# Kernel tuning notes

Hardware: AMD Instinct MI355X
Metric: run time of the kernel (lower is better)

Reference implementation:

```python
import jax, jax.numpy as jnp
import numpy as np

N, E, D, C, G = 100000, 3200000, 128, 10, 512
BN_EPS = 1e-5


def setup_inputs() -> dict:
    key = jax.random.key(0)
    ks = jax.random.split(key, 16)
    s = 0.05
    return {
        "x": jax.random.normal(ks[0], (N, D), jnp.float32),
        "edge_index": jax.random.randint(ks[1], (2, E), 0, N, dtype=jnp.int64),
        "batch": jnp.sort(jax.random.randint(ks[2], (N,), 0, G, dtype=jnp.int64)),
        # 5 stacked GINConv MLPs: Linear->ReLU->Linear->ReLU->BatchNorm
        "conv_W1": jax.random.normal(ks[3], (5, D, D), jnp.float32) * s,
        "conv_b1": jnp.zeros((5, D), jnp.float32),
        "conv_W2": jax.random.normal(ks[4], (5, D, D), jnp.float32) * s,
        "conv_b2": jnp.zeros((5, D), jnp.float32),
        "conv_gamma": jnp.ones((5, D), jnp.float32),
        "conv_beta": jnp.zeros((5, D), jnp.float32),
        # fc1 / fc2: Linear->ReLU->BatchNorm (fc2 is SHARED across stages)
        "fc1_W": jax.random.normal(ks[5], (D, D), jnp.float32) * s,
        "fc1_b": jnp.zeros((D,), jnp.float32),
        "fc1_gamma": jnp.ones((D,), jnp.float32),
        "fc1_beta": jnp.zeros((D,), jnp.float32),
        "fc2_W": jax.random.normal(ks[6], (D, D), jnp.float32) * s,
        "fc2_b": jnp.zeros((D,), jnp.float32),
        "fc2_gamma": jnp.ones((D,), jnp.float32),
        "fc2_beta": jnp.zeros((D,), jnp.float32),
        "lin_W": jax.random.normal(ks[7], (D, C), jnp.float32) * s,
        "lin_b": jnp.zeros((C,), jnp.float32),
    }


def _bn(h, gamma, beta):
    # training-mode BatchNorm1d: batch stats, biased variance
    m = h.mean(axis=0)
    v = h.var(axis=0)
    return (h - m) * jax.lax.rsqrt(v + BN_EPS) * gamma + beta


def _fc(h, W, b, gamma, beta):
    return _bn(jax.nn.relu(h @ W + b), gamma, beta)


def reference(x, edge_index, batch, conv_W1, conv_b1, conv_W2, conv_b2,
              conv_gamma, conv_beta, fc1_W, fc1_b, fc1_gamma, fc1_beta,
              fc2_W, fc2_b, fc2_gamma, fc2_beta, lin_W, lin_b):
    src, dst = edge_index[0], edge_index[1]
    pool = lambda h: jax.ops.segment_sum(h, batch, num_segments=G)

    g = _fc(pool(x), fc1_W, fc1_b, fc1_gamma, fc1_beta)  # x0_g
    total = g
    h = x
    for i in range(5):
        # GINConv, eps=0: nn((1+eps)*x + sum_{j in N(i)} x_j)
        agg = jax.ops.segment_sum(h[src], dst, num_segments=N)
        z = h + agg
        z = jax.nn.relu(z @ conv_W1[i] + conv_b1[i])
        z = jax.nn.relu(z @ conv_W2[i] + conv_b2[i])
        h = _bn(z, conv_gamma[i], conv_beta[i])
        g = _fc(g + pool(h), fc2_W, fc2_b, fc2_gamma, fc2_beta)
        total = total + g
    # dropout omitted (inference); final classifier
    logits = total @ lin_W + lin_b
    return jax.nn.log_softmax(logits, axis=-1)
```

## Files before the change

### kernel.cpp

```cpp
#include <hip/hip_runtime.h>
#include <hip/hip_bf16.h>
#include <math.h>

#define D 128
#define NG 512
#define NC 10
#define PAD 96
#define CAP 704
#define BN_EPS 1e-5f

typedef __attribute__((ext_vector_type(8))) short frag_ab;
typedef __attribute__((ext_vector_type(4))) float f32x4;

__device__ __forceinline__ ushort f2bf(float v) {
    __hip_bfloat16 h = __float2bfloat16(v);
    union { __hip_bfloat16 h; ushort u; } c;
    c.h = h;
    return c.u;
}
__device__ __forceinline__ float bflo(uint u) { return __uint_as_float(u << 16); }
__device__ __forceinline__ float bfhi(uint u) { return __uint_as_float(u & 0xffff0000u); }
__device__ __forceinline__ uint packbf(float x, float y) {
    return (uint)f2bf(x) | ((uint)f2bf(y) << 16);
}

__global__ void zero_ints(int* __restrict__ p, int n) {
    int i = blockIdx.x * blockDim.x + threadIdx.x;
    int s = gridDim.x * blockDim.x;
    for (; i < n; i += s) p[i] = 0;
}

__global__ void scatter_bucket(const int* __restrict__ srcs, const int* __restrict__ dsts, int E,
                               int* __restrict__ bcnt, uint* __restrict__ ebuf) {
    int i = blockIdx.x * blockDim.x + threadIdx.x;
    int s = gridDim.x * blockDim.x;
    for (; i < E; i += s) {
        int d = dsts[i];
        int b = d >> 4;
        int pos = atomicAdd(&bcnt[b], 1);
        if (pos < CAP) ebuf[(size_t)b * CAP + pos] = (uint)srcs[i] | ((uint)(d & 15) << 24);
    }
}

__global__ void csr_phaseB(const uint* __restrict__ ebuf, const int* __restrict__ bcnt,
                           int* __restrict__ cnt, int* __restrict__ pad, int N) {
    int b = blockIdx.x;
    int tid = threadIdx.x;
    int n0 = b << 4;
    __shared__ int lcur[16];
    __shared__ int lpad[16 * PAD];
    if (tid < 16) lcur[tid] = tid * PAD;
    __syncthreads();
    int ec = bcnt[b];
    if (ec > CAP) ec = CAP;
    const uint* eb = ebuf + (size_t)b * CAP;
    for (int e = tid; e < ec; e += 256) {
        uint w = eb[e];
        int ld = w >> 24;
        int pos = atomicAdd(&lcur[ld], 1);
        if (pos < ld * PAD + PAD) lpad[pos] = (int)(w & 0x00FFFFFFu);
    }
    __syncthreads();
    int ne = N - n0;
    if (ne > 16) ne = 16;
    if (tid < ne) {
        int c = lcur[tid] - tid * PAD;
        if (c > PAD) c = PAD;
        cnt[n0 + tid] = c;
    }
    int4* dst4 = (int4*)(pad + (size_t)n0 * PAD);
    const int4* src4l = (const int4*)lpad;
    int tot4 = (ne * PAD) >> 2;
    for (int i = tid; i < tot4; i += 256) dst4[i] = src4l[i];
}

__global__ void gstart_bsearch(const int* __restrict__ batch, int N, int* __restrict__ gstart) {
    int g = blockIdx.x * blockDim.x + threadIdx.x;
    if (g > NG) return;
    if (g == NG) { gstart[NG] = N; return; }
    int lo = 0, hi = N;
    while (lo < hi) {
        int mid = (lo + hi) >> 1;
        if (batch[mid] < g) lo = mid + 1; else hi = mid;
    }
    gstart[g] = lo;
}

__global__ void cvt_bf16(const float* __restrict__ in, uint* __restrict__ out, int nPairs) {
    int i = blockIdx.x * blockDim.x + threadIdx.x;
    int s = gridDim.x * blockDim.x;
    const float2* in2 = (const float2*)in;
    for (; i < nPairs; i += s) {
        float2 v = in2[i];
        out[i] = packbf(v.x, v.y);
    }
}

__global__ void prep_w(const float* __restrict__ W1, const float* __restrict__ W2,
                       ushort* __restrict__ Wt) {
    int m = blockIdx.x;
    const float* W = (m < 5) ? (W1 + (size_t)m * D * D) : (W2 + (size_t)(m - 5) * D * D);
    ushort* out = Wt + (size_t)m * D * D;
    __shared__ ushort ws[D * D];
    int tid = threadIdx.x;
    for (int i = tid; i < D * D; i += 256) ws[i] = f2bf(W[i]);
    __syncthreads();
    int n = tid >> 1, kh = (tid & 1) << 6;
    uint* op = (uint*)(out + n * D + kh);
#pragma unroll 8
    for (int j = 0; j < 32; ++j) {
        uint lo = ws[(kh + 2 * j) * D + n];
        uint hi = ws[(kh + 2 * j + 1) * D + n];
        op[j] = lo | (hi << 16);
    }
}

#define ACC8(V) { s0 += bflo(V.x); s1 += bfhi(V.x); s2 += bflo(V.y); s3 += bfhi(V.y); \
                  s4 += bflo(V.z); s5 += bfhi(V.z); s6 += bflo(V.w); s7 += bfhi(V.w); }

__global__ void agg_pad(const uint4* __restrict__ src4, const float* __restrict__ stats,
                        const float* __restrict__ gamma, const float* __restrict__ beta,
                        float invN, const int* __restrict__ deg, const int* __restrict__ pad,
                        uint4* __restrict__ out4, int N) {
    int gtid = blockIdx.x * blockDim.x + threadIdx.x;
    int grp = gtid >> 4;
    int c16 = gtid & 15;
    int ng = (gridDim.x * blockDim.x) >> 4;
    int cb = c16 * 8;
    float A[8], B[8];
#pragma unroll
    for (int j = 0; j < 8; ++j) { A[j] = 1.f; B[j] = 0.f; }
    if (stats) {
#pragma unroll
        for (int j = 0; j < 8; ++j) {
            int c = cb + j;
            float m = stats[c] * invN;
            float v = fmaxf(stats[D + c] * invN - m * m, 0.f);
            float r = rsqrtf(v + BN_EPS);
            A[j] = r * gamma[c];
            B[j] = beta[c] - m * A[j];
        }
    }
    for (int n = grp; n < N; n += ng) {
        float s0 = 0.f, s1 = 0.f, s2 = 0.f, s3 = 0.f, s4 = 0.f, s5 = 0.f, s6 = 0.f, s7 = 0.f;
        {
            uint4 v = src4[(size_t)n * 16 + c16];
            ACC8(v);
        }
        const int* cp = pad + (size_t)n * PAD;
        int dg = deg[n];
        if (dg > PAD) dg = PAD;
        int e = 0;
        for (; e + 8 <= dg; e += 8) {
            int i0 = cp[e], i1 = cp[e + 1], i2 = cp[e + 2], i3 = cp[e + 3];
            int i4 = cp[e + 4], i5 = cp[e + 5], i6 = cp[e + 6], i7 = cp[e + 7];
            uint4 v0 = src4[(size_t)i0 * 16 + c16];
            uint4 v1 = src4[(size_t)i1 * 16 + c16];
            uint4 v2 = src4[(size_t)i2 * 16 + c16];
            uint4 v3 = src4[(size_t)i3 * 16 + c16];
            uint4 v4 = src4[(size_t)i4 * 16 + c16];
            uint4 v5 = src4[(size_t)i5 * 16 + c16];
            uint4 v6 = src4[(size_t)i6 * 16 + c16];
            uint4 v7 = src4[(size_t)i7 * 16 + c16];
            ACC8(v0); ACC8(v1); ACC8(v2); ACC8(v3);
            ACC8(v4); ACC8(v5); ACC8(v6); ACC8(v7);
        }
        for (; e < dg; ++e) {
            uint4 v0 = src4[(size_t)cp[e] * 16 + c16];
            ACC8(v0);
        }
        float db = (float)(dg + 1);
        uint4 o;
        o.x = packbf(s0 * A[0] + db * B[0], s1 * A[1] + db * B[1]);
        o.y = packbf(s2 * A[2] + db * B[2], s3 * A[3] + db * B[3]);
        o.z = packbf(s4 * A[4] + db * B[4], s5 * A[5] + db * B[5]);
        o.w = packbf(s6 * A[6] + db * B[6], s7 * A[7] + db * B[7]);
        out4[(size_t)n * 16 + c16] = o;
    }
}

__launch_bounds__(256, 2)
__global__ void gin_mlp(const uint* __restrict__ z, const ushort* __restrict__ w1t,
                        const float* __restrict__ b1, const ushort* __restrict__ w2t,
                        const float* __restrict__ b2, uint* __restrict__ outp, int N) {
    int tid = threadIdx.x;
    int lane = tid & 63;
    int wv = tid >> 6;
    int col = lane & 15;
    int kq = lane >> 4;
    int blk = blockIdx.x;
    int m0 = blk * 64 + wv * 16;
    __shared__ __align__(16) ushort cs[64 * D];

    int arow = m0 + col;
    if (arow >= N) arow = N - 1;
    const char* zrow = (const char*)z + (size_t)arow * 256 + kq * 16;
    frag_ab a0 = *(const frag_ab*)(zrow);
    frag_ab a1 = *(const frag_ab*)(zrow + 64);
    frag_ab a2 = *(const frag_ab*)(zrow + 128);
    frag_ab a3 = *(const frag_ab*)(zrow + 192);

    f32x4 acc[8];
#pragma unroll
    for (int n = 0; n < 8; ++n) {
        float bz = b1[n * 16 + col];
        acc[n] = (f32x4){bz, bz, bz, bz};
    }
    const char* wl1 = (const char*)w1t + (size_t)col * 256 + kq * 16;
#pragma unroll
    for (int kc = 0; kc < 4; ++kc) {
        frag_ab av = (kc == 0) ? a0 : (kc == 1) ? a1 : (kc == 2) ? a2 : a3;
#pragma unroll
        for (int n = 0; n < 8; ++n) {
            frag_ab bv = *(const frag_ab*)(wl1 + n * 4096 + kc * 64);
            acc[n] = __builtin_amdgcn_mfma_f32_16x16x32_bf16(av, bv, acc[n], 0, 0, 0);
        }
    }
    int rbase = wv * 16 + kq * 4;
#pragma unroll
    for (int n = 0; n < 8; ++n) {
#pragma unroll
        for (int r = 0; r < 4; ++r) {
            int row = rbase + r;
            int colo = n * 16 + col;
            int chunk = (colo >> 3) ^ (row & 15);
            cs[row * D + chunk * 8 + (colo & 7)] = f2bf(fmaxf(acc[n][r], 0.f));
        }
    }
    __syncthreads();

    int lrow = wv * 16 + col;
    frag_ab c0, c1, c2, c3;
    c0 = *(const frag_ab*)(cs + lrow * D + (((0 << 2) + kq) ^ col) * 8);
    c1 = *(const frag_ab*)(cs + lrow * D + (((1 << 2) + kq) ^ col) * 8);
    c2 = *(const frag_ab*)(cs + lrow * D + (((2 << 2) + kq) ^ col) * 8);
    c3 = *(const frag_ab*)(cs + lrow * D + (((3 << 2) + kq) ^ col) * 8);

#pragma unroll
    for (int n = 0; n < 8; ++n) {
        float bz = b2[n * 16 + col];
        acc[n] = (f32x4){bz, bz, bz, bz};
    }
    const char* wl2 = (const char*)w2t + (size_t)col * 256 + kq * 16;
#pragma unroll
    for (int kc = 0; kc < 4; ++kc) {
        frag_ab av = (kc == 0) ? c0 : (kc == 1) ? c1 : (kc == 2) ? c2 : c3;
#pragma unroll
        for (int n = 0; n < 8; ++n) {
            frag_ab bv = *(const frag_ab*)(wl2 + n * 4096 + kc * 64);
            acc[n] = __builtin_amdgcn_mfma_f32_16x16x32_bf16(av, bv, acc[n], 0, 0, 0);
        }
    }
    __syncthreads();

#pragma unroll
    for (int n = 0; n < 8; ++n) {
#pragma unroll
        for (int r = 0; r < 4; ++r) {
            int row = rbase + r;
            int colo = n * 16 + col;
            int chunk = (colo >> 3) ^ (row & 15);
            cs[row * D + chunk * 8 + (colo & 7)] = f2bf(fmaxf(acc[n][r], 0.f));
        }
    }
    __syncthreads();

    const uint4* csv = (const uint4*)cs;
    uint4* og = (uint4*)outp;
#pragma unroll
    for (int p = 0; p < 4; ++p) {
        int idx = p * 256 + tid;
        int row = idx >> 4;
        int j = idx & 15;
        uint4 v = csv[row * 16 + (j ^ (row & 15))];
        if (blk * 64 + row < N) og[(size_t)blk * 1024 + idx] = v;
    }
}

template <int BF16>
__global__ void pool_stats(const void* __restrict__ zptr, const int* __restrict__ gstart,
                           float* __restrict__ pool, float* __restrict__ stats) {
    int g = blockIdx.x;
    int tid = threadIdx.x;
    int r0 = gstart[g], r1 = gstart[g + 1];
    __shared__ float red[256];
    if (BF16) {
        const uint* z = (const uint*)zptr;
        int uc = tid & 63;
        int qq = tid >> 6;
        float s0 = 0.f, s1 = 0.f, q0 = 0.f, q1 = 0.f;
        for (int r = r0 + qq; r < r1; r += 4) {
            uint u = z[(size_t)r * 64 + uc];
            float lo = bflo(u), hi = bfhi(u);
            s0 += lo; s1 += hi;
            q0 += lo * lo; q1 += hi * hi;
        }
        float S0 = 0.f, S1 = 0.f, Q0 = 0.f, Q1 = 0.f;
        red[tid] = s0; __syncthreads();
        if (qq == 0) S0 = red[uc] + red[uc + 64] + red[uc + 128] + red[uc + 192];
        __syncthreads();
        red[tid] = s1; __syncthreads();
        if (qq == 0) S1 = red[uc] + red[uc + 64] + red[uc + 128] + red[uc + 192];
        __syncthreads();
        red[tid] = q0; __syncthreads();
        if (qq == 0) Q0 = red[uc] + red[uc + 64] + red[uc + 128] + red[uc + 192];
        __syncthreads();
        red[tid] = q1; __syncthreads();
        if (qq == 0) Q1 = red[uc] + red[uc + 64] + red[uc + 128] + red[uc + 192];
        if (qq == 0) {
            pool[g * D + 2 * uc] = S0;
            pool[g * D + 2 * uc + 1] = S1;
            if (stats) {
                atomicAdd(&stats[2 * uc], S0);
                atomicAdd(&stats[2 * uc + 1], S1);
                atomicAdd(&stats[D + 2 * uc], Q0);
                atomicAdd(&stats[D + 2 * uc + 1], Q1);
            }
        }
    } else {
        const float* z = (const float*)zptr;
        int col = tid & 127;
        int half = tid >> 7;
        float s = 0.f;
        for (int r = r0 + half; r < r1; r += 2) s += z[(size_t)r * D + col];
        red[tid] = s;
        __syncthreads();
        if (half == 0) pool[g * D + col] = red[tid] + red[tid + 128];
    }
}

__global__ void fc_forward(const float* __restrict__ pool, const float* __restrict__ stats,
                           const float* __restrict__ gamma, const float* __restrict__ beta,
                           float invN, const int* __restrict__ gstart, const float* __restrict__ gprev,
                           const float* __restrict__ W, const float* __restrict__ bias,
                           float* __restrict__ y, float* __restrict__ ystats) {
    int g = blockIdx.x;
    int tid = threadIdx.x;
    __shared__ float u[D];
    float pv = pool[g * D + tid];
    float uv;
    if (stats) {
        float m = stats[tid] * invN;
        float var = fmaxf(stats[D + tid] * invN - m * m, 0.f);
        float rs = rsqrtf(var + BN_EPS);
        float a = rs * gamma[tid];
        float b = beta[tid] - m * a;
        float cntg = (float)(gstart[g + 1] - gstart[g]);
        uv = gprev[g * D + tid] + pv * a + cntg * b;
    } else {
        uv = pv;
    }
    u[tid] = uv;
    __syncthreads();
    float acc = bias[tid];
#pragma unroll 8
    for (int k = 0; k < D; ++k) acc = fmaf(u[k], W[k * D + tid], acc);
    acc = fmaxf(acc, 0.f);
    y[g * D + tid] = acc;
    atomicAdd(&ystats[tid], acc);
    atomicAdd(&ystats[D + tid], acc * acc);
}

__global__ void fc_bn(const float* __restrict__ y, const float* __restrict__ ystats,
                      const float* __restrict__ gamma, const float* __restrict__ beta,
                      float* __restrict__ gbuf, float* __restrict__ total, int first) {
    int idx = blockIdx.x * blockDim.x + threadIdx.x;
    int d = idx & 127;
    const float invG = 1.f / NG;
    float m = ystats[d] * invG;
    float var = fmaxf(ystats[D + d] * invG - m * m, 0.f);
    float rs = rsqrtf(var + BN_EPS);
    float gv = (y[idx] - m) * rs * gamma[d] + beta[d];
    gbuf[idx] = gv;
    total[idx] = first ? gv : (total[idx] + gv);
}

__global__ void final_logits(const float* __restrict__ total, const float* __restrict__ linW,
                             const float* __restrict__ linb, float* __restrict__ out) {
    int g = blockIdx.x;
    int tid = threadIdx.x;
    __shared__ float t[D];
    __shared__ float lg[12];
    t[tid] = total[g * D + tid];
    __syncthreads();
    if (tid < NC) {
        float a = linb[tid];
        for (int k = 0; k < D; ++k) a = fmaf(t[k], linW[k * NC + tid], a);
        lg[tid] = a;
    }
    __syncthreads();
    if (tid == 0) {
        float mx = lg[0];
        for (int c = 1; c < NC; ++c) mx = fmaxf(mx, lg[c]);
        float se = 0.f;
        for (int c = 0; c < NC; ++c) se += expf(lg[c] - mx);
        lg[10] = mx + logf(se);
    }
    __syncthreads();
    if (tid < NC) out[g * NC + tid] = lg[tid] - lg[10];
}

extern "C" void kernel_launch(void* const* d_in, const int* in_sizes, int n_in,
                              void* d_out, int out_size, void* d_ws, size_t ws_size,
                              hipStream_t stream) {
    const float* x = (const float*)d_in[0];
    const int* edge = (const int*)d_in[1];
    const int* batch = (const int*)d_in[2];
    const float* convW1 = (const float*)d_in[3];
    const float* convb1 = (const float*)d_in[4];
    const float* convW2 = (const float*)d_in[5];
    const float* convb2 = (const float*)d_in[6];
    const float* convgamma = (const float*)d_in[7];
    const float* convbeta = (const float*)d_in[8];
    const float* fc1W = (const float*)d_in[9];
    const float* fc1b = (const float*)d_in[10];
    const float* fc1gamma = (const float*)d_in[11];
    const float* fc1beta = (const float*)d_in[12];
    const float* fc2W = (const float*)d_in[13];
    const float* fc2b = (const float*)d_in[14];
    const float* fc2gamma = (const float*)d_in[15];
    const float* fc2beta = (const float*)d_in[16];
    const float* linW = (const float*)d_in[17];
    const float* linb = (const float*)d_in[18];

    const int N = in_sizes[0] / D;
    const int E = in_sizes[1] / 2;
    const int* srcs = edge;
    const int* dsts = edge + E;
    const float invN = 1.f / (float)N;
    const int NBUK = (N + 15) >> 4;

    char* p = (char*)d_ws;
    auto alloc = [&](size_t bytes) -> void* {
        void* r = (void*)p;
        p += (bytes + 255) & ~(size_t)255;
        return r;
    };
    uint* xb = (uint*)alloc((size_t)N * 64 * 4);
    uint* z  = (uint*)alloc((size_t)N * 64 * 4);
    uint* zB = (uint*)alloc((size_t)N * 64 * 4);
    ushort* wt = (ushort*)alloc((size_t)10 * D * D * 2);
    int* pad = (int*)alloc((size_t)N * PAD * 4);
    int* cnt = (int*)alloc((size_t)N * 4);
    int* gstart = (int*)alloc((size_t)(NG + 1) * 4);
    int zero_n = NBUK + 5 * 2 * D + 6 * 2 * D;
    int* zeroblk = (int*)alloc((size_t)zero_n * 4);
    int* bcnt = zeroblk;
    float* stats_all = (float*)(zeroblk + NBUK);
    float* ystats_all = stats_all + 5 * 2 * D;
    float* pool = (float*)alloc((size_t)NG * D * 4);
    float* ybuf = (float*)alloc((size_t)NG * D * 4);
    float* gbuf = (float*)alloc((size_t)NG * D * 4);
    float* total = (float*)alloc((size_t)NG * D * 4);

    uint* ebuf = z;

    zero_ints<<<(zero_n + 255) / 256, 256, 0, stream>>>(zeroblk, zero_n);
    gstart_bsearch<<<3, 256, 0, stream>>>(batch, N, gstart);
    scatter_bucket<<<2048, 256, 0, stream>>>(srcs, dsts, E, bcnt, ebuf);
    cvt_bf16<<<2048, 256, 0, stream>>>(x, xb, N * 64);
    prep_w<<<10, 256, 0, stream>>>(convW1, convW2, wt);
    csr_phaseB<<<NBUK, 256, 0, stream>>>(ebuf, bcnt, cnt, pad, N);

    pool_stats<0><<<NG, 256, 0, stream>>>(x, gstart, pool, nullptr);
    fc_forward<<<NG, D, 0, stream>>>(pool, nullptr, nullptr, nullptr, 0.f, nullptr, nullptr,
                                     fc1W, fc1b, ybuf, ystats_all);
    fc_bn<<<(NG * D) / 256, 256, 0, stream>>>(ybuf, ystats_all, fc1gamma, fc1beta, gbuf, total, 1);

    const uint* src = xb;
    const int mlp_grid = (N + 63) / 64;
    for (int i = 0; i < 5; ++i) {
        const float* st = (i == 0) ? nullptr : (stats_all + (size_t)(i - 1) * 2 * D);
        const float* ga = (i == 0) ? nullptr : (convgamma + (size_t)(i - 1) * D);
        const float* be = (i == 0) ? nullptr : (convbeta + (size_t)(i - 1) * D);
        agg_pad<<<2048, 256, 0, stream>>>((const uint4*)src, st, ga, be, invN,
                                          cnt, pad, (uint4*)z, N);
        gin_mlp<<<mlp_grid, 256, 0, stream>>>(z, wt + (size_t)i * D * D, convb1 + (size_t)i * D,
                                              wt + (size_t)(5 + i) * D * D, convb2 + (size_t)i * D,
                                              zB, N);
        pool_stats<1><<<NG, 256, 0, stream>>>(zB, gstart, pool, stats_all + (size_t)i * 2 * D);
        float* ys = ystats_all + (size_t)(i + 1) * 2 * D;
        fc_forward<<<NG, D, 0, stream>>>(pool, stats_all + (size_t)i * 2 * D,
                                         convgamma + (size_t)i * D, convbeta + (size_t)i * D,
                                         invN, gstart, gbuf, fc2W, fc2b, ybuf, ys);
        fc_bn<<<(NG * D) / 256, 256, 0, stream>>>(ybuf, ys, fc2gamma, fc2beta, gbuf, total, 0);
        src = zB;
    }

    final_logits<<<NG, D, 0, stream>>>(total, linW, linb, (float*)d_out);
}
```

Measured before the change: 1.586 ms.

## Replace atomic BN statistics with deterministic per-column reductions and trim CSR copy

BatchNorm statistics for the conv outputs and the fc layers were accumulated with global float atomics across 512 graph blocks. They now come from per-graph partial sums written to buffers and reduced by a per-column kernel (col_stats, fc_bn2). fc_bn2 also fuses the fc BatchNorm statistics with the normalization. The CSR pad copy now writes only the filled chunks of each node's neighbor list, which saves write bandwidth. This removes atomic contention and the zeroing of the stats buffers, at the cost of one extra small kernel launch per layer and strided column reads.

```diff
diff --git a/kernel.cpp b/kernel.cpp
--- a/kernel.cpp
+++ b/kernel.cpp
@@ -48,6 +48,7 @@
     int tid = threadIdx.x;
     int n0 = b << 4;
     __shared__ int lcur[16];
+    __shared__ int lcnt2[16];
     __shared__ int lpad[16 * PAD];
     if (tid < 16) lcur[tid] = tid * PAD;
     __syncthreads();
@@ -63,15 +64,20 @@
     __syncthreads();
     int ne = N - n0;
     if (ne > 16) ne = 16;
-    if (tid < ne) {
+    if (tid < 16) {
         int c = lcur[tid] - tid * PAD;
         if (c > PAD) c = PAD;
-        cnt[n0 + tid] = c;
-    }
+        lcnt2[tid] = c;
+    }
+    __syncthreads();
+    if (tid < ne) cnt[n0 + tid] = lcnt2[tid];
+    const int CH = PAD / 4;
     int4* dst4 = (int4*)(pad + (size_t)n0 * PAD);
-    const int4* src4l = (const int4*)lpad;
-    int tot4 = (ne * PAD) >> 2;
-    for (int i = tid; i < tot4; i += 256) dst4[i] = src4l[i];
+    const int4* s4 = (const int4*)lpad;
+    for (int i = tid; i < 16 * CH; i += 256) {
+        int node = i / CH, ch = i - node * CH;
+        if (node < ne && ch * 4 < lcnt2[node]) dst4[node * CH + ch] = s4[node * CH + ch];
+    }
 }
 
 __global__ void gstart_bsearch(const int* __restrict__ batch, int N, int* __restrict__ gstart) {
@@ -279,7 +285,7 @@
 
 template <int BF16>
 __global__ void pool_stats(const void* __restrict__ zptr, const int* __restrict__ gstart,
-                           float* __restrict__ pool, float* __restrict__ stats) {
+                           float* __restrict__ pool, float* __restrict__ sq) {
     int g = blockIdx.x;
     int tid = threadIdx.x;
     int r0 = gstart[g], r1 = gstart[g + 1];
@@ -310,12 +316,8 @@
         if (qq == 0) {
             pool[g * D + 2 * uc] = S0;
             pool[g * D + 2 * uc + 1] = S1;
-            if (stats) {
-                atomicAdd(&stats[2 * uc], S0);
-                atomicAdd(&stats[2 * uc + 1], S1);
-                atomicAdd(&stats[D + 2 * uc], Q0);
-                atomicAdd(&stats[D + 2 * uc + 1], Q1);
-            }
+            sq[g * D + 2 * uc] = Q0;
+            sq[g * D + 2 * uc + 1] = Q1;
         }
     } else {
         const float* z = (const float*)zptr;
@@ -329,11 +331,27 @@
     }
 }
 
+__global__ void col_stats(const float* __restrict__ pool, const float* __restrict__ sq,
+                          float* __restrict__ stats) {
+    int c = blockIdx.x;
+    int tid = threadIdx.x;
+    float s = pool[tid * D + c] + pool[(tid + 256) * D + c];
+    float q = sq[tid * D + c] + sq[(tid + 256) * D + c];
+    __shared__ float rs[256], rq[256];
+    rs[tid] = s; rq[tid] = q;
+    __syncthreads();
+    for (int off = 128; off > 0; off >>= 1) {
+        if (tid < off) { rs[tid] += rs[tid + off]; rq[tid] += rq[tid + off]; }
+        __syncthreads();
+    }
+    if (tid == 0) { stats[c] = rs[0]; stats[D + c] = rq[0]; }
+}
+
 __global__ void fc_forward(const float* __restrict__ pool, const float* __restrict__ stats,
                            const float* __restrict__ gamma, const float* __restrict__ beta,
                            float invN, const int* __restrict__ gstart, const float* __restrict__ gprev,
                            const float* __restrict__ W, const float* __restrict__ bias,
-                           float* __restrict__ y, float* __restrict__ ystats) {
+                           float* __restrict__ y) {
     int g = blockIdx.x;
     int tid = threadIdx.x;
     __shared__ float u[D];
@@ -355,24 +373,40 @@
     float acc = bias[tid];
 #pragma unroll 8
     for (int k = 0; k < D; ++k) acc = fmaf(u[k], W[k * D + tid], acc);
-    acc = fmaxf(acc, 0.f);
-    y[g * D + tid] = acc;
-    atomicAdd(&ystats[tid], acc);
-    atomicAdd(&ystats[D + tid], acc * acc);
-}
-
-__global__ void fc_bn(const float* __restrict__ y, const float* __restrict__ ystats,
-                      const float* __restrict__ gamma, const float* __restrict__ beta,
-                      float* __restrict__ gbuf, float* __restrict__ total, int first) {
-    int idx = blockIdx.x * blockDim.x + threadIdx.x;
-    int d = idx & 127;
-    const float invG = 1.f / NG;
-    float m = ystats[d] * invG;
-    float var = fmaxf(ystats[D + d] * invG - m * m, 0.f);
-    float rs = rsqrtf(var + BN_EPS);
-    float gv = (y[idx] - m) * rs * gamma[d] + beta[d];
-    gbuf[idx] = gv;
-    total[idx] = first ? gv : (total[idx] + gv);
+    y[g * D + tid] = fmaxf(acc, 0.f);
+}
+
+__global__ void fc_bn2(const float* __restrict__ y, const float* __restrict__ gamma,
+                       const float* __restrict__ beta, float* __restrict__ gbuf,
+                       float* __restrict__ total, int first) {
+    int col = blockIdx.x;
+    int tid = threadIdx.x;
+    int i0 = tid * D + col, i1 = (tid + 256) * D + col;
+    float v0 = y[i0], v1 = y[i1];
+    __shared__ float rs[256], rq[256];
+    rs[tid] = v0 + v1;
+    rq[tid] = v0 * v0 + v1 * v1;
+    __syncthreads();
+    for (int off = 128; off > 0; off >>= 1) {
+        if (tid < off) { rs[tid] += rs[tid + off]; rq[tid] += rq[tid + off]; }
+        __syncthreads();
+    }
+    __shared__ float ab[2];
+    if (tid == 0) {
+        const float invG = 1.f / NG;
+        float m = rs[0] * invG;
+        float var = fmaxf(rq[0] * invG - m * m, 0.f);
+        float a = rsqrtf(var + BN_EPS) * gamma[col];
+        ab[0] = a;
+        ab[1] = beta[col] - m * a;
+    }
+    __syncthreads();
+    float a = ab[0], b = ab[1];
+    float g0 = v0 * a + b, g1 = v1 * a + b;
+    gbuf[i0] = g0;
+    gbuf[i1] = g1;
+    if (first) { total[i0] = g0; total[i1] = g1; }
+    else { total[i0] += g0; total[i1] += g1; }
 }
 
 __global__ void final_logits(const float* __restrict__ total, const float* __restrict__ linW,
@@ -443,19 +477,17 @@
     int* pad = (int*)alloc((size_t)N * PAD * 4);
     int* cnt = (int*)alloc((size_t)N * 4);
     int* gstart = (int*)alloc((size_t)(NG + 1) * 4);
-    int zero_n = NBUK + 5 * 2 * D + 6 * 2 * D;
-    int* zeroblk = (int*)alloc((size_t)zero_n * 4);
-    int* bcnt = zeroblk;
-    float* stats_all = (float*)(zeroblk + NBUK);
-    float* ystats_all = stats_all + 5 * 2 * D;
+    int* bcnt = (int*)alloc((size_t)NBUK * 4);
+    float* stats_all = (float*)alloc((size_t)5 * 2 * D * 4);
     float* pool = (float*)alloc((size_t)NG * D * 4);
+    float* sqbuf = (float*)alloc((size_t)NG * D * 4);
     float* ybuf = (float*)alloc((size_t)NG * D * 4);
     float* gbuf = (float*)alloc((size_t)NG * D * 4);
     float* total = (float*)alloc((size_t)NG * D * 4);
 
     uint* ebuf = z;
 
-    zero_ints<<<(zero_n + 255) / 256, 256, 0, stream>>>(zeroblk, zero_n);
+    zero_ints<<<(NBUK + 255) / 256, 256, 0, stream>>>(bcnt, NBUK);
     gstart_bsearch<<<3, 256, 0, stream>>>(batch, N, gstart);
     scatter_bucket<<<2048, 256, 0, stream>>>(srcs, dsts, E, bcnt, ebuf);
     cvt_bf16<<<2048, 256, 0, stream>>>(x, xb, N * 64);
@@ -464,8 +496,8 @@
 
     pool_stats<0><<<NG, 256, 0, stream>>>(x, gstart, pool, nullptr);
     fc_forward<<<NG, D, 0, stream>>>(pool, nullptr, nullptr, nullptr, 0.f, nullptr, nullptr,
-                                     fc1W, fc1b, ybuf, ystats_all);
-    fc_bn<<<(NG * D) / 256, 256, 0, stream>>>(ybuf, ystats_all, fc1gamma, fc1beta, gbuf, total, 1);
+                                     fc1W, fc1b, ybuf);
+    fc_bn2<<<D, 256, 0, stream>>>(ybuf, fc1gamma, fc1beta, gbuf, total, 1);
 
     const uint* src = xb;
     const int mlp_grid = (N + 63) / 64;
@@ -478,12 +510,13 @@
         gin_mlp<<<mlp_grid, 256, 0, stream>>>(z, wt + (size_t)i * D * D, convb1 + (size_t)i * D,
                                               wt + (size_t)(5 + i) * D * D, convb2 + (size_t)i * D,
                                               zB, N);
-        pool_stats<1><<<NG, 256, 0, stream>>>(zB, gstart, pool, stats_all + (size_t)i * 2 * D);
-        float* ys = ystats_all + (size_t)(i + 1) * 2 * D;
-        fc_forward<<<NG, D, 0, stream>>>(pool, stats_all + (size_t)i * 2 * D,
+        float* st_i = stats_all + (size_t)i * 2 * D;
+        pool_stats<1><<<NG, 256, 0, stream>>>(zB, gstart, pool, sqbuf);
+        col_stats<<<D, 256, 0, stream>>>(pool, sqbuf, st_i);
+        fc_forward<<<NG, D, 0, stream>>>(pool, st_i,
                                          convgamma + (size_t)i * D, convbeta + (size_t)i * D,
-                                         invN, gstart, gbuf, fc2W, fc2b, ybuf, ys);
-        fc_bn<<<(NG * D) / 256, 256, 0, stream>>>(ybuf, ys, fc2gamma, fc2beta, gbuf, total, 0);
+                                         invN, gstart, gbuf, fc2W, fc2b, ybuf);
+        fc_bn2<<<D, 256, 0, stream>>>(ybuf, fc2gamma, fc2beta, gbuf, total, 0);
         src = zB;
     }
 
```

Result: faster. 1.392 ms (-12.2%).
